# Optimization experiments

Hardware: AMD Instinct MI355X
Metric: run time of the kernel (lower is better)

Reference implementation:

```python
import jax, jax.numpy as jnp
import numpy as np

H = 512
TEMPERATURE = 1.0


def setup_inputs() -> dict:
    key = jax.random.key(0)
    ks = jax.random.split(key, 9)
    B, Q, S = 4, 64, 1024
    scale = 1.0 / np.sqrt(H)
    return {
        "query": jax.random.normal(ks[0], (B, Q, H), jnp.float32),
        "key_": jax.random.normal(ks[1], (B, S, H), jnp.float32),
        "value": jax.random.normal(ks[2], (B, S, H), jnp.float32),
        "Wq": jax.random.normal(ks[3], (H, H), jnp.float32) * scale,
        "bq": jax.random.normal(ks[4], (H,), jnp.float32) * 0.01,
        "Wk": jax.random.normal(ks[5], (H, H), jnp.float32) * scale,
        "bk": jax.random.normal(ks[6], (H,), jnp.float32) * 0.01,
        "we": jax.random.normal(ks[7], (H,), jnp.float32) * scale,
        "be": jax.random.normal(ks[8], (), jnp.float32) * 0.01,
    }


def reference(query, key_, value, Wq, bq, Wk, bk, we, be):
    # query: [B,Q,H], key_/value: [B,S,H]
    qp = jnp.einsum("bqd,dh->bqh", query, Wq) + bq          # [B,Q,H]
    kp = jnp.einsum("bsd,dh->bsh", key_, Wk) + bk           # [B,S,H]
    attn_sum = jnp.tanh(qp[:, :, None, :] + kp[:, None, :, :])  # [B,Q,S,H]
    scores = (jnp.einsum("bqsh,h->bqs", attn_sum, we) + be) / TEMPERATURE
    weights = jax.nn.softmax(scores, axis=-1)               # [B,Q,S]
    context = jnp.einsum("bqs,bsh->bqh", weights, value)    # [B,Q,H]
    return context, weights
```

## Files before the change

kernel.cpp:

```cpp
#include <hip/hip_runtime.h>


constexpr int kB = 4;
constexpr int kQ = 64;
constexpr int kS = 1024;
constexpr int kH = 512;

typedef short bf16x8 __attribute__((ext_vector_type(8)));
typedef float f32x4 __attribute__((ext_vector_type(4)));

__device__ __forceinline__ unsigned bf16rtn_bits(float x) {
  unsigned u = __float_as_uint(x);
  u += 0x7FFFu + ((u >> 16) & 1u);
  return u;
}

__global__ __launch_bounds__(256) void convert_w(
    const float* __restrict__ Wk, const float* __restrict__ Wq,
    unsigned short* __restrict__ Bhi, unsigned short* __restrict__ Blo) {
  const int gid = blockIdx.x * 256 + threadIdx.x;
  const int c = gid & 63;
  const int g = (gid >> 6) & 3;
  const int kt = (gid >> 8) & 15;
  const int ct = (gid >> 12) & 7;
  const int mat = gid >> 15;
  const float* W = mat ? Wq : Wk;
  const float* src = W + (size_t)(kt * 32 + g * 8) * kH + ct * 64 + c;
  bf16x8 hv, lv;
#pragma unroll
  for (int j = 0; j < 8; j++) {
    float x = src[(size_t)j * kH];
    unsigned u = bf16rtn_bits(x);
    float hf = __uint_as_float(u & 0xFFFF0000u);
    unsigned v = bf16rtn_bits(x - hf);
    hv[j] = (short)(u >> 16);
    lv[j] = (short)(v >> 16);
  }
  *(bf16x8*)(Bhi + (size_t)gid * 8) = hv;
  *(bf16x8*)(Blo + (size_t)gid * 8) = lv;
}

__global__ __launch_bounds__(256) void proj_mfma(
    const float* __restrict__ key_, const float* __restrict__ query,
    const unsigned short* __restrict__ Bhi, const unsigned short* __restrict__ Blo,
    const float* __restrict__ bk, const float* __restrict__ bq,
    float* __restrict__ kp, float* __restrict__ qp) {
  __shared__ __align__(16) unsigned short AhiL[2][2048];
  __shared__ __align__(16) unsigned short AloL[2][2048];
  __shared__ __align__(16) unsigned short BhiL[2][2048];
  __shared__ __align__(16) unsigned short BloL[2][2048];

  const int ct = blockIdx.x;
  int rt = blockIdx.y;
  const float* X;
  const float* bias;
  float* Y;
  int mat;
  if (rt < 64) {
    X = key_ + (size_t)rt * 64 * kH; bias = bk; Y = kp + (size_t)rt * 64 * kH; mat = 0;
  } else {
    rt -= 64;
    X = query + (size_t)rt * 64 * kH; bias = bq; Y = qp + (size_t)rt * 64 * kH; mat = 1;
  }

  const int t = threadIdx.x;
  const int ar = t & 63, ag = t >> 6;
  const float* aptr = X + (size_t)ar * kH + ag * 8;
  const unsigned short* bht = Bhi + ((size_t)(mat * 8 + ct) * 16) * 2048 + t * 8;
  const unsigned short* blt = Blo + ((size_t)(mat * 8 + ct) * 16) * 2048 + t * 8;

  float4 pa0, pa1;
  uint4 pbh, pbl;
  auto gload = [&](int kt) {
    const float* p = aptr + kt * 32;
    pa0 = *(const float4*)p;
    pa1 = *(const float4*)(p + 4);
    pbh = *(const uint4*)(bht + (size_t)kt * 2048);
    pbl = *(const uint4*)(blt + (size_t)kt * 2048);
  };
  auto cwrite = [&](int buf) {
    bf16x8 hv, lv;
#define CVT1(x, e)                                          \
  {                                                         \
    unsigned u = bf16rtn_bits(x);                           \
    float hf = __uint_as_float(u & 0xFFFF0000u);            \
    unsigned v = bf16rtn_bits((x) - hf);                    \
    hv[e] = (short)(u >> 16);                               \
    lv[e] = (short)(v >> 16);                               \
  }
    CVT1(pa0.x, 0) CVT1(pa0.y, 1) CVT1(pa0.z, 2) CVT1(pa0.w, 3)
    CVT1(pa1.x, 4) CVT1(pa1.y, 5) CVT1(pa1.z, 6) CVT1(pa1.w, 7)
#undef CVT1
    *(bf16x8*)&AhiL[buf][t * 8] = hv;
    *(bf16x8*)&AloL[buf][t * 8] = lv;
    *(uint4*)&BhiL[buf][t * 8] = pbh;
    *(uint4*)&BloL[buf][t * 8] = pbl;
  };

  const int l = t & 63, lg = l >> 4, lr = l & 15;
  const int wv = t >> 6, wm = wv >> 1, wn = wv & 1;
  const int oa0 = (lg * 64 + (2 * wm) * 16 + lr) * 8;
  const int ob0 = (lg * 64 + (2 * wn) * 16 + lr) * 8;

  f32x4 acc00 = {0.f, 0.f, 0.f, 0.f};
  f32x4 acc01 = acc00, acc10 = acc00, acc11 = acc00;

  gload(0);
  cwrite(0);
  __syncthreads();

#pragma unroll 2
  for (int kt = 0; kt < 16; kt++) {
    if (kt < 15) gload(kt + 1);

    const unsigned short* Ah = AhiL[kt & 1];
    const unsigned short* Al = AloL[kt & 1];
    const unsigned short* Bh = BhiL[kt & 1];
    const unsigned short* Bl = BloL[kt & 1];
    bf16x8 ah0 = *(const bf16x8*)(Ah + oa0);
    bf16x8 ah1 = *(const bf16x8*)(Ah + oa0 + 128);
    bf16x8 al0 = *(const bf16x8*)(Al + oa0);
    bf16x8 al1 = *(const bf16x8*)(Al + oa0 + 128);
    bf16x8 bh0 = *(const bf16x8*)(Bh + ob0);
    bf16x8 bh1 = *(const bf16x8*)(Bh + ob0 + 128);
    bf16x8 bl0 = *(const bf16x8*)(Bl + ob0);
    bf16x8 bl1 = *(const bf16x8*)(Bl + ob0 + 128);

    acc00 = __builtin_amdgcn_mfma_f32_16x16x32_bf16(ah0, bh0, acc00, 0, 0, 0);
    acc01 = __builtin_amdgcn_mfma_f32_16x16x32_bf16(ah0, bh1, acc01, 0, 0, 0);
    acc10 = __builtin_amdgcn_mfma_f32_16x16x32_bf16(ah1, bh0, acc10, 0, 0, 0);
    acc11 = __builtin_amdgcn_mfma_f32_16x16x32_bf16(ah1, bh1, acc11, 0, 0, 0);
    acc00 = __builtin_amdgcn_mfma_f32_16x16x32_bf16(al0, bh0, acc00, 0, 0, 0);
    acc01 = __builtin_amdgcn_mfma_f32_16x16x32_bf16(al0, bh1, acc01, 0, 0, 0);
    acc10 = __builtin_amdgcn_mfma_f32_16x16x32_bf16(al1, bh0, acc10, 0, 0, 0);
    acc11 = __builtin_amdgcn_mfma_f32_16x16x32_bf16(al1, bh1, acc11, 0, 0, 0);
    acc00 = __builtin_amdgcn_mfma_f32_16x16x32_bf16(ah0, bl0, acc00, 0, 0, 0);
    acc01 = __builtin_amdgcn_mfma_f32_16x16x32_bf16(ah0, bl1, acc01, 0, 0, 0);
    acc10 = __builtin_amdgcn_mfma_f32_16x16x32_bf16(ah1, bl0, acc10, 0, 0, 0);
    acc11 = __builtin_amdgcn_mfma_f32_16x16x32_bf16(ah1, bl1, acc11, 0, 0, 0);

    if (kt < 15) {
      cwrite((kt + 1) & 1);
      __syncthreads();
    }
  }

  const int n0 = ct * 64;
  const int col0 = n0 + (2 * wn) * 16 + lr;
  const float b0 = bias[col0];
  const float b1 = bias[col0 + 16];
  const int row0 = (2 * wm) * 16 + lg * 4;
#pragma unroll
  for (int jj = 0; jj < 4; jj++) {
    float* y = Y + (size_t)(row0 + jj) * kH;
    y[col0]      = 2.f * (acc00[jj] + b0);
    y[col0 + 16] = 2.f * (acc01[jj] + b1);
    float* y2 = y + (size_t)16 * kH;
    y2[col0]      = 2.f * (acc10[jj] + b0);
    y2[col0 + 16] = 2.f * (acc11[jj] + b1);
  }
}

__global__ __launch_bounds__(256) void score_kernel(
    const float* __restrict__ qp, const float* __restrict__ kp,
    const float* __restrict__ we, float* __restrict__ sout) {
  const int bx = blockIdx.x;
  const int b = bx >> 8, qt = (bx >> 4) & 15, st = bx & 15;
  const int t = threadIdx.x, wave = t >> 6, lane = t & 63;

  const float4* we4 = (const float4*)(we + lane * 8);
  float4 w0 = we4[0], w1 = we4[1];
  float wsum = w0.x + w0.y + w0.z + w0.w + w1.x + w1.y + w1.z + w1.w;
#pragma unroll
  for (int off = 32; off; off >>= 1) wsum += __shfl_xor(wsum, off);
  w0.x *= -2.f; w0.y *= -2.f; w0.z *= -2.f; w0.w *= -2.f;
  w1.x *= -2.f; w1.y *= -2.f; w1.z *= -2.f; w1.w *= -2.f;

  const int q0 = qt * 4;
  float4 qv[4][2];
#pragma unroll
  for (int i = 0; i < 4; i++) {
    const float4* q4 = (const float4*)(qp + (size_t)(b * kQ + q0 + i) * kH + lane * 8);
    qv[i][0] = q4[0]; qv[i][1] = q4[1];
  }

  const int sbase = st * 64 + wave * 16;
  const float* kbase = kp + ((size_t)b * kS + sbase) * kH + lane * 8;

  float4 k0 = *(const float4*)(kbase);
  float4 k1 = *(const float4*)(kbase + 4);

  for (int si = 0; si < 16; si++) {
    float4 n0, n1;
    if (si < 15) {
      const float* np = kbase + (size_t)(si + 1) * kH;
      n0 = *(const float4*)(np);
      n1 = *(const float4*)(np + 4);
    }
    float a[4];
#pragma unroll
    for (int i = 0; i < 4; i++) {
      float acc = 0.f, e;
      e = __expf(qv[i][0].x + k0.x); acc = fmaf(w0.x, __builtin_amdgcn_rcpf(1.f + e), acc);
      e = __expf(qv[i][0].y + k0.y); acc = fmaf(w0.y, __builtin_amdgcn_rcpf(1.f + e), acc);
      e = __expf(qv[i][0].z + k0.z); acc = fmaf(w0.z, __builtin_amdgcn_rcpf(1.f + e), acc);
      e = __expf(qv[i][0].w + k0.w); acc = fmaf(w0.w, __builtin_amdgcn_rcpf(1.f + e), acc);
      e = __expf(qv[i][1].x + k1.x); acc = fmaf(w1.x, __builtin_amdgcn_rcpf(1.f + e), acc);
      e = __expf(qv[i][1].y + k1.y); acc = fmaf(w1.y, __builtin_amdgcn_rcpf(1.f + e), acc);
      e = __expf(qv[i][1].z + k1.z); acc = fmaf(w1.z, __builtin_amdgcn_rcpf(1.f + e), acc);
      e = __expf(qv[i][1].w + k1.w); acc = fmaf(w1.w, __builtin_amdgcn_rcpf(1.f + e), acc);
      a[i] = acc;
    }
#pragma unroll
    for (int i = 0; i < 4; i++) {
#pragma unroll
      for (int off = 32; off; off >>= 1) a[i] += __shfl_xor(a[i], off);
    }
    if (lane == 0) {
      const int s = sbase + si;
#pragma unroll
      for (int i = 0; i < 4; i++)
        sout[(size_t)(b * kQ + q0 + i) * kS + s] = a[i] + wsum;
    }
    k0 = n0; k1 = n1;
  }
}

__global__ __launch_bounds__(256) void softmax_kernel(float* __restrict__ wout) {
  __shared__ float redm[4];
  __shared__ float reds[4];
  const int row = blockIdx.x;
  const int t = threadIdx.x, wave = t >> 6, lane = t & 63;
  float4* rp = (float4*)(wout + (size_t)row * kS);
  float4 v = rp[t];

  float m = fmaxf(fmaxf(v.x, v.y), fmaxf(v.z, v.w));
#pragma unroll
  for (int off = 32; off; off >>= 1) m = fmaxf(m, __shfl_xor(m, off));
  if (lane == 0) redm[wave] = m;
  __syncthreads();
  m = fmaxf(fmaxf(redm[0], redm[1]), fmaxf(redm[2], redm[3]));

  float4 e;
  e.x = __expf(v.x - m); e.y = __expf(v.y - m);
  e.z = __expf(v.z - m); e.w = __expf(v.w - m);
  float sum = e.x + e.y + e.z + e.w;
#pragma unroll
  for (int off = 32; off; off >>= 1) sum += __shfl_xor(sum, off);
  if (lane == 0) reds[wave] = sum;
  __syncthreads();
  sum = reds[0] + reds[1] + reds[2] + reds[3];
  float inv = 1.f / sum;
  e.x *= inv; e.y *= inv; e.z *= inv; e.w *= inv;
  rp[t] = e;
}

__global__ __launch_bounds__(256) void context_kernel(
    const float* __restrict__ wout, const float* __restrict__ value,
    float* __restrict__ part) {
  __shared__ __align__(16) float wt[128][16];
  const int bx = blockIdx.x;
  const int sc = bx & 7, qc = (bx >> 3) & 3, hc = (bx >> 5) & 1, b = bx >> 6;
  const int t = threadIdx.x;
  const int s0 = sc * 128, q0 = qc * 16;

  {
    const int q_l = t & 15;
    const int sseg = (t >> 4) * 8;
    const float4* p4 =
        (const float4*)(wout + (size_t)(b * kQ + q0 + q_l) * kS + s0 + sseg);
    float4 u0 = p4[0], u1 = p4[1];
    wt[sseg + 0][q_l] = u0.x; wt[sseg + 1][q_l] = u0.y;
    wt[sseg + 2][q_l] = u0.z; wt[sseg + 3][q_l] = u0.w;
    wt[sseg + 4][q_l] = u1.x; wt[sseg + 5][q_l] = u1.y;
    wt[sseg + 6][q_l] = u1.z; wt[sseg + 7][q_l] = u1.w;
  }
  __syncthreads();

  const int h = hc * 256 + t;
  const float* vb = value + ((size_t)b * kS + s0) * kH + h;
  float acc[16];
#pragma unroll
  for (int i = 0; i < 16; i++) acc[i] = 0.f;

#pragma unroll 4
  for (int s = 0; s < 128; s++) {
    float v = vb[(size_t)s * kH];
    const float4* wrow = (const float4*)&wt[s][0];
    float4 a0 = wrow[0], a1 = wrow[1], a2 = wrow[2], a3 = wrow[3];
    acc[0]  = fmaf(a0.x, v, acc[0]);  acc[1]  = fmaf(a0.y, v, acc[1]);
    acc[2]  = fmaf(a0.z, v, acc[2]);  acc[3]  = fmaf(a0.w, v, acc[3]);
    acc[4]  = fmaf(a1.x, v, acc[4]);  acc[5]  = fmaf(a1.y, v, acc[5]);
    acc[6]  = fmaf(a1.z, v, acc[6]);  acc[7]  = fmaf(a1.w, v, acc[7]);
    acc[8]  = fmaf(a2.x, v, acc[8]);  acc[9]  = fmaf(a2.y, v, acc[9]);
    acc[10] = fmaf(a2.z, v, acc[10]); acc[11] = fmaf(a2.w, v, acc[11]);
    acc[12] = fmaf(a3.x, v, acc[12]); acc[13] = fmaf(a3.y, v, acc[13]);
    acc[14] = fmaf(a3.z, v, acc[14]); acc[15] = fmaf(a3.w, v, acc[15]);
  }

  float* pp = part + (size_t)sc * kB * kQ * kH;
#pragma unroll
  for (int i = 0; i < 16; i++)
    pp[(size_t)(b * kQ + q0 + i) * kH + h] = acc[i];
}

__global__ __launch_bounds__(256) void reduce_kernel(
    const float* __restrict__ part, float* __restrict__ ctx) {
  const int i = blockIdx.x * 256 + threadIdx.x;
  float4 a = {0, 0, 0, 0};
#pragma unroll
  for (int p = 0; p < 8; p++) {
    float4 v = ((const float4*)(part + (size_t)p * kB * kQ * kH))[i];
    a.x += v.x; a.y += v.y; a.z += v.z; a.w += v.w;
  }
  ((float4*)ctx)[i] = a;
}

extern "C" void kernel_launch(void* const* d_in, const int* in_sizes, int n_in,
                              void* d_out, int out_size, void* d_ws,
                              size_t ws_size, hipStream_t stream) {
  const float* query = (const float*)d_in[0];
  const float* key_  = (const float*)d_in[1];
  const float* value = (const float*)d_in[2];
  const float* Wq    = (const float*)d_in[3];
  const float* bq    = (const float*)d_in[4];
  const float* Wk    = (const float*)d_in[5];
  const float* bk    = (const float*)d_in[6];
  const float* we    = (const float*)d_in[7];

  float* ctx  = (float*)d_out;
  float* wout = (float*)d_out + (size_t)kB * kQ * kH;

  float* qp   = (float*)d_ws;
  float* kp   = qp + (size_t)kB * kQ * kH;
  float* part = kp;
  unsigned short* Bhi =
      (unsigned short*)((char*)d_ws + (size_t)(kB * kQ * kH + kB * kS * kH) * 4);
  unsigned short* Blo = Bhi + (size_t)2 * 8 * 16 * 256 * 8;

  convert_w<<<256, 256, 0, stream>>>(Wk, Wq, Bhi, Blo);
  proj_mfma<<<dim3(8, 68), 256, 0, stream>>>(key_, query, Bhi, Blo, bk, bq, kp, qp);
  score_kernel<<<1024, 256, 0, stream>>>(qp, kp, we, wout);
  softmax_kernel<<<kB * kQ, 256, 0, stream>>>(wout);
  context_kernel<<<256, 256, 0, stream>>>(wout, value, part);
  reduce_kernel<<<kB * kQ * kH / 4 / 256, 256, 0, stream>>>(part, ctx);
}
```

Before: 157.3 us.

## Precompute exp of projections and factor tanh into products in score kernel

The projection kernel now stores exp(2*(xW+b)) instead of 2*(xW+b). The score kernel can then form exp(2(q+k)) as a product Eq*Ek with no per-element exp. The score kernel is restructured to tile K rows through double-buffered, XOR-swizzled LDS while query rows and weights stay in shared memory. Each thread produces one score per query directly, removing the wave-wide shuffle reductions, and pairs of terms are combined so that one reciprocal serves two elements. The cost is possible overflow or precision loss when the exponentials grow large, which random inputs with magnitudes around unit scale are unlikely to reach.

```diff
diff --git a/kernel.cpp b/kernel.cpp
--- a/kernel.cpp
+++ b/kernel.cpp
@@ -44,7 +44,7 @@
     const float* __restrict__ key_, const float* __restrict__ query,
     const unsigned short* __restrict__ Bhi, const unsigned short* __restrict__ Blo,
     const float* __restrict__ bk, const float* __restrict__ bq,
-    float* __restrict__ kp, float* __restrict__ qp) {
+    float* __restrict__ Ek, float* __restrict__ Eq) {
   __shared__ __align__(16) unsigned short AhiL[2][2048];
   __shared__ __align__(16) unsigned short AloL[2][2048];
   __shared__ __align__(16) unsigned short BhiL[2][2048];
@@ -57,10 +57,10 @@
   float* Y;
   int mat;
   if (rt < 64) {
-    X = key_ + (size_t)rt * 64 * kH; bias = bk; Y = kp + (size_t)rt * 64 * kH; mat = 0;
+    X = key_ + (size_t)rt * 64 * kH; bias = bk; Y = Ek + (size_t)rt * 64 * kH; mat = 0;
   } else {
     rt -= 64;
-    X = query + (size_t)rt * 64 * kH; bias = bq; Y = qp + (size_t)rt * 64 * kH; mat = 1;
+    X = query + (size_t)rt * 64 * kH; bias = bq; Y = Eq + (size_t)rt * 64 * kH; mat = 1;
   }
 
   const int t = threadIdx.x;
@@ -71,12 +71,12 @@
 
   float4 pa0, pa1;
   uint4 pbh, pbl;
-  auto gload = [&](int kt) {
-    const float* p = aptr + kt * 32;
+  auto gload = [&](int kt2) {
+    const float* p = aptr + kt2 * 32;
     pa0 = *(const float4*)p;
     pa1 = *(const float4*)(p + 4);
-    pbh = *(const uint4*)(bht + (size_t)kt * 2048);
-    pbl = *(const uint4*)(blt + (size_t)kt * 2048);
+    pbh = *(const uint4*)(bht + (size_t)kt2 * 2048);
+    pbl = *(const uint4*)(blt + (size_t)kt2 * 2048);
   };
   auto cwrite = [&](int buf) {
     bf16x8 hv, lv;
@@ -110,13 +110,13 @@
   __syncthreads();
 
 #pragma unroll 2
-  for (int kt = 0; kt < 16; kt++) {
-    if (kt < 15) gload(kt + 1);
-
-    const unsigned short* Ah = AhiL[kt & 1];
-    const unsigned short* Al = AloL[kt & 1];
-    const unsigned short* Bh = BhiL[kt & 1];
-    const unsigned short* Bl = BloL[kt & 1];
+  for (int kt2 = 0; kt2 < 16; kt2++) {
+    if (kt2 < 15) gload(kt2 + 1);
+
+    const unsigned short* Ah = AhiL[kt2 & 1];
+    const unsigned short* Al = AloL[kt2 & 1];
+    const unsigned short* Bh = BhiL[kt2 & 1];
+    const unsigned short* Bl = BloL[kt2 & 1];
     bf16x8 ah0 = *(const bf16x8*)(Ah + oa0);
     bf16x8 ah1 = *(const bf16x8*)(Ah + oa0 + 128);
     bf16x8 al0 = *(const bf16x8*)(Al + oa0);
@@ -139,8 +139,8 @@
     acc10 = __builtin_amdgcn_mfma_f32_16x16x32_bf16(ah1, bl0, acc10, 0, 0, 0);
     acc11 = __builtin_amdgcn_mfma_f32_16x16x32_bf16(ah1, bl1, acc11, 0, 0, 0);
 
-    if (kt < 15) {
-      cwrite((kt + 1) & 1);
+    if (kt2 < 15) {
+      cwrite((kt2 + 1) & 1);
       __syncthreads();
     }
   }
@@ -153,77 +153,111 @@
 #pragma unroll
   for (int jj = 0; jj < 4; jj++) {
     float* y = Y + (size_t)(row0 + jj) * kH;
-    y[col0]      = 2.f * (acc00[jj] + b0);
-    y[col0 + 16] = 2.f * (acc01[jj] + b1);
+    y[col0]      = __expf(2.f * (acc00[jj] + b0));
+    y[col0 + 16] = __expf(2.f * (acc01[jj] + b1));
     float* y2 = y + (size_t)16 * kH;
-    y2[col0]      = 2.f * (acc10[jj] + b0);
-    y2[col0 + 16] = 2.f * (acc11[jj] + b1);
+    y2[col0]      = __expf(2.f * (acc10[jj] + b0));
+    y2[col0 + 16] = __expf(2.f * (acc11[jj] + b1));
   }
 }
 
 __global__ __launch_bounds__(256) void score_kernel(
-    const float* __restrict__ qp, const float* __restrict__ kp,
+    const float* __restrict__ Eq, const float* __restrict__ Ek,
     const float* __restrict__ we, float* __restrict__ sout) {
-  const int bx = blockIdx.x;
-  const int b = bx >> 8, qt = (bx >> 4) & 15, st = bx & 15;
-  const int t = threadIdx.x, wave = t >> 6, lane = t & 63;
+  __shared__ __align__(16) float EkL[2][64 * 64];
+  __shared__ __align__(16) float EqL[8 * 512];
+  __shared__ __align__(16) float wL[512];
+
+  const int qt = blockIdx.x, st = blockIdx.y, b = blockIdx.z;
+  const int t = threadIdx.x, wv = t >> 6, lane = t & 63;
+  const int s0 = st * 64;
+  const int q0g = b * kQ + qt * 8;
+  const int qA = wv * 2;
 
   const float4* we4 = (const float4*)(we + lane * 8);
-  float4 w0 = we4[0], w1 = we4[1];
-  float wsum = w0.x + w0.y + w0.z + w0.w + w1.x + w1.y + w1.z + w1.w;
+  float4 u0 = we4[0], u1 = we4[1];
+  float wsum = u0.x + u0.y + u0.z + u0.w + u1.x + u1.y + u1.z + u1.w;
 #pragma unroll
   for (int off = 32; off; off >>= 1) wsum += __shfl_xor(wsum, off);
-  w0.x *= -2.f; w0.y *= -2.f; w0.z *= -2.f; w0.w *= -2.f;
-  w1.x *= -2.f; w1.y *= -2.f; w1.z *= -2.f; w1.w *= -2.f;
-
-  const int q0 = qt * 4;
-  float4 qv[4][2];
-#pragma unroll
-  for (int i = 0; i < 4; i++) {
-    const float4* q4 = (const float4*)(qp + (size_t)(b * kQ + q0 + i) * kH + lane * 8);
-    qv[i][0] = q4[0]; qv[i][1] = q4[1];
-  }
-
-  const int sbase = st * 64 + wave * 16;
-  const float* kbase = kp + ((size_t)b * kS + sbase) * kH + lane * 8;
-
-  float4 k0 = *(const float4*)(kbase);
-  float4 k1 = *(const float4*)(kbase + 4);
-
-  for (int si = 0; si < 16; si++) {
-    float4 n0, n1;
-    if (si < 15) {
-      const float* np = kbase + (size_t)(si + 1) * kH;
-      n0 = *(const float4*)(np);
-      n1 = *(const float4*)(np + 4);
-    }
-    float a[4];
+
+  if (t < 128) {
+    float4 w = ((const float4*)we)[t];
+    w.x *= -2.f; w.y *= -2.f; w.z *= -2.f; w.w *= -2.f;
+    ((float4*)wL)[t] = w;
+  }
+  {
+    const float4* src = (const float4*)(Eq + (size_t)q0g * kH);
 #pragma unroll
     for (int i = 0; i < 4; i++) {
-      float acc = 0.f, e;
-      e = __expf(qv[i][0].x + k0.x); acc = fmaf(w0.x, __builtin_amdgcn_rcpf(1.f + e), acc);
-      e = __expf(qv[i][0].y + k0.y); acc = fmaf(w0.y, __builtin_amdgcn_rcpf(1.f + e), acc);
-      e = __expf(qv[i][0].z + k0.z); acc = fmaf(w0.z, __builtin_amdgcn_rcpf(1.f + e), acc);
-      e = __expf(qv[i][0].w + k0.w); acc = fmaf(w0.w, __builtin_amdgcn_rcpf(1.f + e), acc);
-      e = __expf(qv[i][1].x + k1.x); acc = fmaf(w1.x, __builtin_amdgcn_rcpf(1.f + e), acc);
-      e = __expf(qv[i][1].y + k1.y); acc = fmaf(w1.y, __builtin_amdgcn_rcpf(1.f + e), acc);
-      e = __expf(qv[i][1].z + k1.z); acc = fmaf(w1.z, __builtin_amdgcn_rcpf(1.f + e), acc);
-      e = __expf(qv[i][1].w + k1.w); acc = fmaf(w1.w, __builtin_amdgcn_rcpf(1.f + e), acc);
-      a[i] = acc;
-    }
+      int idx = t + 256 * i;
+      ((float4*)EqL)[idx] = src[idx];
+    }
+  }
+
+  const int er = t >> 4;
+  const int ej = t & 15;
+  const float* ekg = Ek + (size_t)(b * kS + s0 + er) * kH + ej * 4;
+  float4 pk[4];
+  auto gload = [&](int c) {
+#pragma unroll
+    for (int i = 0; i < 4; i++)
+      pk[i] = *(const float4*)(ekg + (size_t)(16 * i) * kH + c * 64);
+  };
+  auto lwrite = [&](int buf) {
 #pragma unroll
     for (int i = 0; i < 4; i++) {
-#pragma unroll
-      for (int off = 32; off; off >>= 1) a[i] += __shfl_xor(a[i], off);
-    }
-    if (lane == 0) {
-      const int s = sbase + si;
-#pragma unroll
-      for (int i = 0; i < 4; i++)
-        sout[(size_t)(b * kQ + q0 + i) * kS + s] = a[i] + wsum;
-    }
-    k0 = n0; k1 = n1;
-  }
+      const int row = er + 16 * i;
+      *(float4*)(&EkL[buf][row * 64 + ((ej ^ (row & 15)) << 2)]) = pk[i];
+    }
+  };
+
+  gload(0);
+  lwrite(0);
+  __syncthreads();
+
+  float accA = 0.f, accB = 0.f;
+  const int sw = lane & 15;
+  const float* eqa = EqL + (qA + 0) * 512;
+  const float* eqb = EqL + (qA + 1) * 512;
+
+  for (int c = 0; c < 8; c++) {
+    if (c < 7) gload(c + 1);
+    const float* ekb = &EkL[c & 1][lane * 64];
+    const float* wc = wL + c * 64;
+    const float* ea = eqa + c * 64;
+    const float* eb = eqb + c * 64;
+#pragma unroll 4
+    for (int g = 0; g < 16; g++) {
+      float4 ek = *(const float4*)(ekb + ((g ^ sw) << 2));
+      float4 w = *(const float4*)(wc + g * 4);
+      float4 qa = *(const float4*)(ea + g * 4);
+      float4 qb = *(const float4*)(eb + g * 4);
+      {
+        float a1 = fmaf(qa.x, ek.x, 1.f), b1 = fmaf(qa.y, ek.y, 1.f);
+        float n1 = fmaf(w.y, a1, w.x * b1);
+        accA = fmaf(n1, __builtin_amdgcn_rcpf(a1 * b1), accA);
+        float a2 = fmaf(qa.z, ek.z, 1.f), b2 = fmaf(qa.w, ek.w, 1.f);
+        float n2 = fmaf(w.w, a2, w.z * b2);
+        accA = fmaf(n2, __builtin_amdgcn_rcpf(a2 * b2), accA);
+      }
+      {
+        float a1 = fmaf(qb.x, ek.x, 1.f), b1 = fmaf(qb.y, ek.y, 1.f);
+        float n1 = fmaf(w.y, a1, w.x * b1);
+        accB = fmaf(n1, __builtin_amdgcn_rcpf(a1 * b1), accB);
+        float a2 = fmaf(qb.z, ek.z, 1.f), b2 = fmaf(qb.w, ek.w, 1.f);
+        float n2 = fmaf(w.w, a2, w.z * b2);
+        accB = fmaf(n2, __builtin_amdgcn_rcpf(a2 * b2), accB);
+      }
+    }
+    if (c < 7) {
+      __syncthreads();
+      lwrite((c + 1) & 1);
+      __syncthreads();
+    }
+  }
+
+  sout[(size_t)(q0g + qA + 0) * kS + s0 + lane] = accA + wsum;
+  sout[(size_t)(q0g + qA + 1) * kS + s0 + lane] = accB + wsum;
 }
 
 __global__ __launch_bounds__(256) void softmax_kernel(float* __restrict__ wout) {
@@ -331,16 +365,16 @@
   float* ctx  = (float*)d_out;
   float* wout = (float*)d_out + (size_t)kB * kQ * kH;
 
-  float* qp   = (float*)d_ws;
-  float* kp   = qp + (size_t)kB * kQ * kH;
-  float* part = kp;
+  float* Eq   = (float*)d_ws;
+  float* Ek   = Eq + (size_t)kB * kQ * kH;
+  float* part = Ek;
   unsigned short* Bhi =
       (unsigned short*)((char*)d_ws + (size_t)(kB * kQ * kH + kB * kS * kH) * 4);
   unsigned short* Blo = Bhi + (size_t)2 * 8 * 16 * 256 * 8;
 
   convert_w<<<256, 256, 0, stream>>>(Wk, Wq, Bhi, Blo);
-  proj_mfma<<<dim3(8, 68), 256, 0, stream>>>(key_, query, Bhi, Blo, bk, bq, kp, qp);
-  score_kernel<<<1024, 256, 0, stream>>>(qp, kp, we, wout);
+  proj_mfma<<<dim3(8, 68), 256, 0, stream>>>(key_, query, Bhi, Blo, bk, bq, Ek, Eq);
+  score_kernel<<<dim3(8, 16, 4), 256, 0, stream>>>(Eq, Ek, we, wout);
   softmax_kernel<<<kB * kQ, 256, 0, stream>>>(wout);
   context_kernel<<<256, 256, 0, stream>>>(wout, value, part);
   reduce_kernel<<<kB * kQ * kH / 4 / 256, 256, 0, stream>>>(part, ctx);
```

Result: faster. 150.1 us (-4.6%).
